# Kernel tuning notes

Hardware: AMD Instinct MI355X
Metric: run time of the kernel (lower is better)

The kernel has to match this reference:

```python
import math
import jax, jax.numpy as jnp
import numpy as np

N_HEADS = 16
NUM_BUCKETS = 32
MAX_DISTANCE = 128
ROTARY_BASE = 10000.0


def rotate_half(x):
    x1, x2 = jnp.split(x, 2, axis=-1)
    return jnp.concatenate((-x2, x1), axis=-1)


def rotary_freqs(T, dim):
    inv_freq = 1.0 / (ROTARY_BASE ** (jnp.arange(0, dim, 2, dtype=jnp.float32) / dim))
    t = jnp.arange(T, dtype=jnp.float32)
    freqs = jnp.einsum('i,j->ij', t, inv_freq)  # [T, dim/2]
    return jnp.concatenate((freqs, freqs), axis=-1)  # [T, dim]


def rel_pos_bucket_causal(rel_pos, num_buckets=NUM_BUCKETS, max_distance=MAX_DISTANCE):
    n = jnp.maximum(-rel_pos, 0)  # [T, T] int
    max_exact = num_buckets // 2
    is_small = n < max_exact
    n_safe = jnp.maximum(n, 1).astype(jnp.float32)
    val_if_large = max_exact + (
        jnp.log(n_safe / max_exact) / math.log(max_distance / max_exact) * (num_buckets - max_exact)
    ).astype(jnp.int32)
    val_if_large = jnp.minimum(val_if_large, num_buckets - 1)
    return jnp.where(is_small, n, val_if_large)


def setup_inputs() -> dict:
    key = jax.random.key(0)
    ks = jax.random.split(key, 10)
    B, T, C = 2, 2048, 1024
    s = 0.02
    return {
        'x':  jax.random.normal(ks[0], (B, T, C), dtype=jnp.float32),
        'Wq': jax.random.normal(ks[1], (C, C), dtype=jnp.float32) * s,
        'bq': jnp.zeros((C,), dtype=jnp.float32),
        'Wk': jax.random.normal(ks[2], (C, C), dtype=jnp.float32) * s,
        'bk': jnp.zeros((C,), dtype=jnp.float32),
        'Wv': jax.random.normal(ks[3], (C, C), dtype=jnp.float32) * s,
        'bv': jnp.zeros((C,), dtype=jnp.float32),
        'Wp': jax.random.normal(ks[4], (C, C), dtype=jnp.float32) * s,
        'bp': jnp.zeros((C,), dtype=jnp.float32),
        'rel_bias_table': jax.random.normal(ks[5], (NUM_BUCKETS, N_HEADS), dtype=jnp.float32) * s,
    }


def reference(x, Wq, bq, Wk, bk, Wv, bv, Wp, bp, rel_bias_table):
    B, T, C = x.shape
    H = N_HEADS
    D = C // H

    def heads(y):
        return y.reshape(B, T, H, D).transpose(0, 2, 1, 3)  # [B,H,T,D]

    q = heads(x @ Wq + bq)
    k = heads(x @ Wk + bk)
    v = heads(x @ Wv + bv)

    # rotary (use_xpos=False -> scale=1)
    freqs = rotary_freqs(T, D)  # [T, D]
    cos, sin = jnp.cos(freqs), jnp.sin(freqs)
    q = q * cos + rotate_half(q) * sin
    k = k * cos + rotate_half(k) * sin

    # relative position bias (causal, scale=1.0)
    pos = jnp.arange(T)
    rel_pos = pos[None, :] - pos[:, None]  # k_pos - q_pos
    bucket = rel_pos_bucket_causal(rel_pos)  # [T, T]
    bias = rel_bias_table[bucket]  # [T, T, H]
    bias = bias.transpose(2, 0, 1)  # [H, T, T]

    att = jnp.einsum('bhid,bhjd->bhij', q, k) + bias[None]
    att = att * (1.0 / math.sqrt(D))
    causal = pos[None, :] <= pos[:, None]  # tril mask [T, T]
    att = jnp.where(causal[None, None], att, -jnp.inf)
    att = jax.nn.softmax(att, axis=-1)

    y = jnp.einsum('bhij,bhjd->bhid', att, v)  # [B,H,T,D]
    y = y.transpose(0, 2, 1, 3).reshape(B, T, C)
    return y @ Wp + bp
```

## Files before the change

### kernel.cpp

```cpp
#include <hip/hip_runtime.h>
#include <hip/hip_bf16.h>
#include <math.h>

#define B_ 2
#define T_ 2048
#define C_ 1024
#define H_ 16
#define D_ 64
#define M_ (B_ * T_)
#define K_ 1024

#define SCALE2 0.18033688011112043f

typedef short bf16x8 __attribute__((ext_vector_type(8)));
typedef float f32x4  __attribute__((ext_vector_type(4)));
typedef unsigned int u32;

__device__ __forceinline__ float u2f(unsigned short u) {
    union { unsigned int i; float f; } v; v.i = ((unsigned int)u) << 16; return v.f;
}
__device__ __forceinline__ unsigned short f2b(float f) {
    __hip_bfloat16 h = __float2bfloat16(f);
    return *reinterpret_cast<unsigned short*>(&h);
}
__device__ __forceinline__ u32 pack_bf16_rnd(float a, float b) {
    const u32 au = __float_as_uint(a) + 0x8000u;
    const u32 bu = __float_as_uint(b) + 0x8000u;
    return __builtin_amdgcn_perm(bu, au, 0x07060302u);
}
__device__ __forceinline__ void load_lds16(const void* g, void* l) {
    __builtin_amdgcn_global_load_lds(
        (const __attribute__((address_space(1))) u32*)g,
        (__attribute__((address_space(3))) u32*)l, 16, 0, 0);
}

__global__ __launch_bounds__(256) void prep(
    const float* __restrict__ x,
    const float* __restrict__ W0, const float* __restrict__ W1,
    const float* __restrict__ W2, const float* __restrict__ W3,
    const float* __restrict__ tbl,
    unsigned short* __restrict__ xb,
    unsigned short* __restrict__ T0, unsigned short* __restrict__ T1,
    unsigned short* __restrict__ T2, unsigned short* __restrict__ T3,
    float* __restrict__ dtab, float2* __restrict__ trig)
{
    __shared__ __align__(16) unsigned short tile[64][72];
    const int bx = blockIdx.x;
    const int tid = threadIdx.x;

    if (bx < 2048) {
        const int idx = bx * 256 + tid;
        const float4 a = reinterpret_cast<const float4*>(x)[idx * 2];
        const float4 b = reinterpret_cast<const float4*>(x)[idx * 2 + 1];
        unsigned short t[8] = {f2b(a.x), f2b(a.y), f2b(a.z), f2b(a.w),
                               f2b(b.x), f2b(b.y), f2b(b.z), f2b(b.w)};
        reinterpret_cast<bf16x8*>(xb)[idx] = *reinterpret_cast<const bf16x8*>(t);
    } else if (bx < 3072) {
        const int w = bx - 2048;
        const int z = w >> 8;
        const int rem = w & 255;
        const int k0 = (rem & 15) * 64, n0 = (rem >> 4) * 64;
        const float* W = z == 0 ? W0 : z == 1 ? W1 : z == 2 ? W2 : W3;
        unsigned short* Wt = z == 0 ? T0 : z == 1 ? T1 : z == 2 ? T2 : T3;

        #pragma unroll
        for (int it = 0; it < 4; ++it) {
            const int idx = it * 256 + tid;
            const int r = idx >> 4, c = (idx & 15) * 4;
            const float4 w4 = *reinterpret_cast<const float4*>(W + (size_t)(k0 + r) * C_ + n0 + c);
            tile[r][c + 0] = f2b(w4.x); tile[r][c + 1] = f2b(w4.y);
            tile[r][c + 2] = f2b(w4.z); tile[r][c + 3] = f2b(w4.w);
        }
        __syncthreads();
        #pragma unroll
        for (int it = 0; it < 2; ++it) {
            const int idx = it * 256 + tid;
            const int nc = idx >> 3, kc = (idx & 7) * 8;
            unsigned short tmp[8];
            #pragma unroll
            for (int e = 0; e < 8; ++e) tmp[e] = tile[kc + e][nc];
            *reinterpret_cast<bf16x8*>(Wt + (size_t)(n0 + nc) * K_ + k0 + kc) =
                *reinterpret_cast<const bf16x8*>(tmp);
        }
    } else {
        const int idx = (bx - 3072) * 256 + tid;
        if (idx < H_ * T_) {
            const int h = idx >> 11, n = idx & (T_ - 1);
            int bucket;
            if (n < 16) bucket = n;
            else {
                int vb = 16 + (int)(log2f((float)n * 0.0625f) * (16.0f / 3.0f));
                bucket = vb < 31 ? vb : 31;
            }
            dtab[idx] = tbl[bucket * H_ + h] * SCALE2;
        }
        const int t = idx >> 5, j = idx & 31;
        const float inv = exp2f(-(float)j * (13.287712379549449f / 32.0f));
        const float ang = (float)t * inv;
        trig[idx] = make_float2(cosf(ang), sinf(ang));
    }
}

__device__ __forceinline__ void gemm_core(
    const unsigned short* __restrict__ A, const unsigned short* __restrict__ Bt,
    const float* __restrict__ bias, const float2* __restrict__ trig,
    float rot_scale, float* __restrict__ outf,
    unsigned short* __restrict__ outb, int mode)
{
    __shared__ __align__(16) unsigned short As[128 * 32];
    __shared__ __align__(16) unsigned short Bs[128 * 32];

    const int tid = threadIdx.x;
    const int wid = tid >> 6, lane = tid & 63;
    const int l16 = lane & 15, quad = lane >> 4;
    const int wm = wid >> 1, wn = wid & 1;
    const int m0 = blockIdx.y * 128, n0 = blockIdx.x * 128;

    f32x4 acc[4][4];
    #pragma unroll
    for (int i = 0; i < 4; ++i)
        #pragma unroll
        for (int j = 0; j < 4; ++j) acc[i][j] = (f32x4){0.f, 0.f, 0.f, 0.f};

    char* AsB = (char*)As;
    char* BsB = (char*)Bs;

    for (int k0 = 0; k0 < K_; k0 += 32) {
        __syncthreads();
        #pragma unroll
        for (int it = 0; it < 2; ++it) {
            const int idx = it * 256 + tid;
            const int row = idx >> 2, ch = (idx & 3) * 8;
            const int ldso = it * 4096 + wid * 1024;
            load_lds16(A + (size_t)(m0 + row) * K_ + k0 + ch, AsB + ldso);
            load_lds16(Bt + (size_t)(n0 + row) * K_ + k0 + ch, BsB + ldso);
        }
        __syncthreads();

        bf16x8 af[4], bf[4];
        #pragma unroll
        for (int i = 0; i < 4; ++i) {
            af[i] = *reinterpret_cast<const bf16x8*>(&As[(wm * 64 + i * 16 + l16) * 32 + quad * 8]);
            bf[i] = *reinterpret_cast<const bf16x8*>(&Bs[(wn * 64 + i * 16 + l16) * 32 + quad * 8]);
        }
        #pragma unroll
        for (int i = 0; i < 4; ++i)
            #pragma unroll
            for (int j = 0; j < 4; ++j)
                acc[i][j] = __builtin_amdgcn_mfma_f32_16x16x32_bf16(af[i], bf[j], acc[i][j], 0, 0, 0);
    }

    if (mode == 1) {
        #pragma unroll
        for (int i = 0; i < 4; ++i) {
            const int mb = m0 + wm * 64 + i * 16 + quad * 4;
            const int bb = mb >> 11, tb = mb & (T_ - 1);
            #pragma unroll
            for (int jc = 0; jc < 2; ++jc) {
                const int n_lo = n0 + wn * 64 + jc * 16 + l16;
                const int h = n_lo >> 6, d = n_lo & 63;
                const float bv_lo = bias[n_lo], bv_hi = bias[n_lo + 32];
                unsigned short* po = outb + (((size_t)bb * H_ + h) * T_ + tb) * D_ + d;
                #pragma unroll
                for (int r = 0; r < 4; ++r) {
                    const float2 cs = trig[(tb + r) * 32 + d];
                    const float a = acc[i][jc][r] + bv_lo;
                    const float b = acc[i][jc + 2][r] + bv_hi;
                    po[(size_t)r * D_]      = f2b((a * cs.x - b * cs.y) * rot_scale);
                    po[(size_t)r * D_ + 32] = f2b((b * cs.x + a * cs.y) * rot_scale);
                }
            }
        }
        return;
    }

    #pragma unroll
    for (int i = 0; i < 4; ++i) {
        const int mb = m0 + wm * 64 + i * 16 + quad * 4;
        #pragma unroll
        for (int j = 0; j < 4; ++j) {
            const int n = n0 + wn * 64 + j * 16 + l16;
            const float bv = bias[n];
            if (mode == 2) {
                const int bb = mb >> 11, t = mb & (T_ - 1);
                const int h = n >> 6, d = n & 63;
                uint2 w;
                w.x = pack_bf16_rnd(acc[i][j][0] + bv, acc[i][j][1] + bv);
                w.y = pack_bf16_rnd(acc[i][j][2] + bv, acc[i][j][3] + bv);
                *reinterpret_cast<uint2*>(
                    outb + (((size_t)bb * H_ + h) * D_ + d) * T_ + t) = w;
            } else {
                #pragma unroll
                for (int r = 0; r < 4; ++r)
                    outf[(size_t)(mb + r) * C_ + n] = acc[i][j][r] + bv;
            }
        }
    }
}

__global__ __launch_bounds__(256) void gemm_qkv(
    const unsigned short* __restrict__ A,
    const unsigned short* __restrict__ Wq, const unsigned short* __restrict__ Wk,
    const unsigned short* __restrict__ Wv,
    const float* __restrict__ bq, const float* __restrict__ bk,
    const float* __restrict__ bv, const float2* __restrict__ trig,
    unsigned short* __restrict__ Qo, unsigned short* __restrict__ Ko,
    unsigned short* __restrict__ Vto)
{
    const int z = blockIdx.z;
    const unsigned short* Bt = z == 0 ? Wq : z == 1 ? Wk : Wv;
    const float* bias = z == 0 ? bq : z == 1 ? bk : bv;
    unsigned short* outb = z == 0 ? Qo : z == 1 ? Ko : Vto;
    const float rs = z == 0 ? SCALE2 : 1.0f;
    gemm_core(A, Bt, bias, trig, rs, nullptr, outb, z == 2 ? 2 : 1);
}

__global__ __launch_bounds__(256) void gemm_proj(
    const unsigned short* __restrict__ A, const unsigned short* __restrict__ Bt,
    const float* __restrict__ bias, float* __restrict__ outf)
{
    gemm_core(A, Bt, bias, nullptr, 1.0f, outf, nullptr, 0);
}

__global__ __launch_bounds__(256) void flash_attn(
    const unsigned short* __restrict__ Q, const unsigned short* __restrict__ K,
    const unsigned short* __restrict__ Vt, const float* __restrict__ dtab,
    unsigned short* __restrict__ Y)
{
    __shared__ __align__(16) unsigned short Ks[64][72];
    __shared__ __align__(16) unsigned short Vs[64][72];
    __shared__ __align__(16) unsigned short Ps[4][16][72];
    __shared__ float bias_ls[64 + T_];

    const int bh = blockIdx.y;
    const int qt = (int)((blockIdx.x + blockIdx.y) & 31);
    const int h = bh & (H_ - 1), b = bh >> 4;
    const int tid = threadIdx.x;
    const int wid = tid >> 6, lane = tid & 63;
    const int l16 = lane & 15, quad = lane >> 4;
    const size_t base = (size_t)bh * T_ * D_;
    const size_t vbase = (size_t)bh * D_ * T_;
    const int q0 = qt * 64;

    if (tid < 64) bias_ls[tid] = -INFINITY;
    for (int ii = tid; ii < q0 + 64; ii += 256) bias_ls[64 + ii] = dtab[h * T_ + ii];

    bf16x8 ones;
    #pragma unroll
    for (int e = 0; e < 8; ++e) ones[e] = (short)0x3F80;

    const int arow = q0 + wid * 16 + l16;
    const int crow = q0 + wid * 16 + quad * 4;
    const int nbase = crow - l16 * 4;

    const int sr0 = tid >> 3,         sch0 = (tid & 7) * 8;
    const int sr1 = (tid + 256) >> 3, sch1 = ((tid + 256) & 7) * 8;

    bf16x8 qf[2];
    qf[0] = *reinterpret_cast<const bf16x8*>(Q + base + (size_t)arow * D_ + quad * 8);
    qf[1] = *reinterpret_cast<const bf16x8*>(Q + base + (size_t)arow * D_ + 32 + quad * 8);

    bf16x8 kr[2], vr[2];
    kr[0] = *reinterpret_cast<const bf16x8*>(K + base + (size_t)sr0 * D_ + sch0);
    kr[1] = *reinterpret_cast<const bf16x8*>(K + base + (size_t)sr1 * D_ + sch1);
    vr[0] = *reinterpret_cast<const bf16x8*>(Vt + vbase + (size_t)sr0 * T_ + sch0);
    vr[1] = *reinterpret_cast<const bf16x8*>(Vt + vbase + (size_t)sr1 * T_ + sch1);

    f32x4 o[4], ol;
    #pragma unroll
    for (int c = 0; c < 4; ++c) o[c] = (f32x4){0.f, 0.f, 0.f, 0.f};
    ol = (f32x4){0.f, 0.f, 0.f, 0.f};

    for (int kt = 0; kt <= qt; ++kt) {
        const int j0 = kt * 64;
        __syncthreads();

        *reinterpret_cast<bf16x8*>(&Ks[sr0][sch0]) = kr[0];
        *reinterpret_cast<bf16x8*>(&Ks[sr1][sch1]) = kr[1];
        *reinterpret_cast<bf16x8*>(&Vs[sr0][sch0]) = vr[0];
        *reinterpret_cast<bf16x8*>(&Vs[sr1][sch1]) = vr[1];
        __syncthreads();

        if (kt < qt) {
            const int j1 = j0 + 64;
            kr[0] = *reinterpret_cast<const bf16x8*>(K + base + (size_t)(j1 + sr0) * D_ + sch0);
            kr[1] = *reinterpret_cast<const bf16x8*>(K + base + (size_t)(j1 + sr1) * D_ + sch1);
            vr[0] = *reinterpret_cast<const bf16x8*>(Vt + vbase + (size_t)sr0 * T_ + j1 + sch0);
            vr[1] = *reinterpret_cast<const bf16x8*>(Vt + vbase + (size_t)sr1 * T_ + j1 + sch1);
        }

        f32x4 sc[4];
        #pragma unroll
        for (int c = 0; c < 4; ++c) sc[c] = (f32x4){0.f, 0.f, 0.f, 0.f};
        #pragma unroll
        for (int c = 0; c < 4; ++c) {
            #pragma unroll
            for (int s = 0; s < 2; ++s) {
                bf16x8 kf = *reinterpret_cast<const bf16x8*>(
                    &Ks[l16 * 4 + c][s * 32 + quad * 8]);
                sc[c] = __builtin_amdgcn_mfma_f32_16x16x32_bf16(qf[s], kf, sc[c], 0, 0, 0);
            }
        }

        #pragma unroll
        for (int r = 0; r < 4; ++r) {
            const float* bp0 = &bias_ls[64 + nbase - j0 + r];
            const float p0 = exp2f(sc[0][r] + bp0[0]);
            const float p1 = exp2f(sc[1][r] + bp0[-1]);
            const float p2 = exp2f(sc[2][r] + bp0[-2]);
            const float p3 = exp2f(sc[3][r] + bp0[-3]);
            uint2 w;
            w.x = pack_bf16_rnd(p0, p1);
            w.y = pack_bf16_rnd(p2, p3);
            *reinterpret_cast<uint2*>(&Ps[wid][quad * 4 + r][l16 * 4]) = w;
        }

        #pragma unroll
        for (int s = 0; s < 2; ++s) {
            bf16x8 pf = *reinterpret_cast<const bf16x8*>(&Ps[wid][l16][s * 32 + quad * 8]);
            #pragma unroll
            for (int c = 0; c < 4; ++c) {
                bf16x8 vf = *reinterpret_cast<const bf16x8*>(&Vs[c * 16 + l16][s * 32 + quad * 8]);
                o[c] = __builtin_amdgcn_mfma_f32_16x16x32_bf16(pf, vf, o[c], 0, 0, 0);
            }
            ol = __builtin_amdgcn_mfma_f32_16x16x32_bf16(pf, ones, ol, 0, 0, 0);
        }
    }

    #pragma unroll
    for (int r = 0; r < 4; ++r) {
        const int i = crow + r;
        const float invl = 1.0f / ol[r];
        #pragma unroll
        for (int c = 0; c < 4; ++c)
            Y[((size_t)b * T_ + i) * C_ + h * D_ + c * 16 + l16] = f2b(o[c][r] * invl);
    }
}

extern "C" void kernel_launch(void* const* d_in, const int* in_sizes, int n_in,
                              void* d_out, int out_size, void* d_ws, size_t ws_size,
                              hipStream_t stream)
{
    const float* x   = (const float*)d_in[0];
    const float* Wq  = (const float*)d_in[1];
    const float* bq  = (const float*)d_in[2];
    const float* Wk  = (const float*)d_in[3];
    const float* bk  = (const float*)d_in[4];
    const float* Wv  = (const float*)d_in[5];
    const float* bv  = (const float*)d_in[6];
    const float* Wp  = (const float*)d_in[7];
    const float* bp  = (const float*)d_in[8];
    const float* tbl = (const float*)d_in[9];
    float* out = (float*)d_out;

    const size_t n1 = (size_t)B_ * H_ * T_ * D_;
    const size_t nW = (size_t)C_ * C_;
    unsigned short* xb  = (unsigned short*)d_ws;
    unsigned short* Wqt = xb + (size_t)M_ * K_;
    unsigned short* Wkt = Wqt + nW;
    unsigned short* Wvt = Wkt + nW;
    unsigned short* Wpt = Wvt + nW;
    unsigned short* Qb  = Wpt + nW;
    unsigned short* Kb  = Qb + n1;
    unsigned short* Vtb = Kb + n1;
    unsigned short* Yb  = Vtb + n1;
    float* dtab = (float*)(Yb + n1);
    float2* trig = (float2*)(dtab + H_ * T_);

    const dim3 blk(256);

    prep<<<dim3(3328), blk, 0, stream>>>(x, Wq, Wk, Wv, Wp, tbl,
                                         xb, Wqt, Wkt, Wvt, Wpt, dtab, trig);

    gemm_qkv<<<dim3(C_ / 128, M_ / 128, 3), blk, 0, stream>>>(
        xb, Wqt, Wkt, Wvt, bq, bk, bv, trig, Qb, Kb, Vtb);

    flash_attn<<<dim3(32, B_ * H_), blk, 0, stream>>>(Qb, Kb, Vtb, dtab, Yb);

    gemm_proj<<<dim3(C_ / 128, M_ / 128), blk, 0, stream>>>(Yb, Wpt, bp, out);
}
```

Baseline: 212.8 us.

## Pair causal query tiles per block and fold bias into MFMA accumulator

Each attention block now handles two query tiles (qt and 31-qt), so every block does the same amount of causal work and the grid shrinks from 32 to 16 blocks per head. The relative-position bias is loaded as vectors and used to initialise the QK^T accumulator, which removes the per-element bias adds before exp2. s_setprio is raised around the MFMA sections. The cost is fewer blocks (512) and therefore less parallelism, plus a serial second pass within each block that starts by reloading the first K/V tile.

After: 213.6 us. No clear change (+0.4%).

```diff
diff --git a/kernel.cpp b/kernel.cpp
--- a/kernel.cpp
+++ b/kernel.cpp
@@ -230,35 +230,28 @@
     __shared__ __align__(16) unsigned short Ks[64][72];
     __shared__ __align__(16) unsigned short Vs[64][72];
     __shared__ __align__(16) unsigned short Ps[4][16][72];
-    __shared__ float bias_ls[64 + T_];
+    __shared__ __align__(16) float bias_ls[64 + T_];
 
     const int bh = blockIdx.y;
-    const int qt = (int)((blockIdx.x + blockIdx.y) & 31);
     const int h = bh & (H_ - 1), b = bh >> 4;
     const int tid = threadIdx.x;
     const int wid = tid >> 6, lane = tid & 63;
     const int l16 = lane & 15, quad = lane >> 4;
     const size_t base = (size_t)bh * T_ * D_;
     const size_t vbase = (size_t)bh * D_ * T_;
-    const int q0 = qt * 64;
+
+    const int qta = (int)((blockIdx.x + blockIdx.y) & 15);
+    const int qtb = 31 - qta;
 
     if (tid < 64) bias_ls[tid] = -INFINITY;
-    for (int ii = tid; ii < q0 + 64; ii += 256) bias_ls[64 + ii] = dtab[h * T_ + ii];
+    for (int ii = tid; ii < qtb * 64 + 64; ii += 256) bias_ls[64 + ii] = dtab[h * T_ + ii];
 
     bf16x8 ones;
     #pragma unroll
     for (int e = 0; e < 8; ++e) ones[e] = (short)0x3F80;
 
-    const int arow = q0 + wid * 16 + l16;
-    const int crow = q0 + wid * 16 + quad * 4;
-    const int nbase = crow - l16 * 4;
-
     const int sr0 = tid >> 3,         sch0 = (tid & 7) * 8;
     const int sr1 = (tid + 256) >> 3, sch1 = ((tid + 256) & 7) * 8;
-
-    bf16x8 qf[2];
-    qf[0] = *reinterpret_cast<const bf16x8*>(Q + base + (size_t)arow * D_ + quad * 8);
-    qf[1] = *reinterpret_cast<const bf16x8*>(Q + base + (size_t)arow * D_ + 32 + quad * 8);
 
     bf16x8 kr[2], vr[2];
     kr[0] = *reinterpret_cast<const bf16x8*>(K + base + (size_t)sr0 * D_ + sch0);
@@ -266,74 +259,102 @@
     vr[0] = *reinterpret_cast<const bf16x8*>(Vt + vbase + (size_t)sr0 * T_ + sch0);
     vr[1] = *reinterpret_cast<const bf16x8*>(Vt + vbase + (size_t)sr1 * T_ + sch1);
 
-    f32x4 o[4], ol;
-    #pragma unroll
-    for (int c = 0; c < 4; ++c) o[c] = (f32x4){0.f, 0.f, 0.f, 0.f};
-    ol = (f32x4){0.f, 0.f, 0.f, 0.f};
-
-    for (int kt = 0; kt <= qt; ++kt) {
-        const int j0 = kt * 64;
-        __syncthreads();
-
-        *reinterpret_cast<bf16x8*>(&Ks[sr0][sch0]) = kr[0];
-        *reinterpret_cast<bf16x8*>(&Ks[sr1][sch1]) = kr[1];
-        *reinterpret_cast<bf16x8*>(&Vs[sr0][sch0]) = vr[0];
-        *reinterpret_cast<bf16x8*>(&Vs[sr1][sch1]) = vr[1];
-        __syncthreads();
-
-        if (kt < qt) {
-            const int j1 = j0 + 64;
-            kr[0] = *reinterpret_cast<const bf16x8*>(K + base + (size_t)(j1 + sr0) * D_ + sch0);
-            kr[1] = *reinterpret_cast<const bf16x8*>(K + base + (size_t)(j1 + sr1) * D_ + sch1);
-            vr[0] = *reinterpret_cast<const bf16x8*>(Vt + vbase + (size_t)sr0 * T_ + j1 + sch0);
-            vr[1] = *reinterpret_cast<const bf16x8*>(Vt + vbase + (size_t)sr1 * T_ + j1 + sch1);
-        }
-
-        f32x4 sc[4];
-        #pragma unroll
-        for (int c = 0; c < 4; ++c) sc[c] = (f32x4){0.f, 0.f, 0.f, 0.f};
-        #pragma unroll
-        for (int c = 0; c < 4; ++c) {
+    for (int qi = 0; qi < 2; ++qi) {
+        const int qt = qi ? qta : qtb;
+        const int q0 = qt * 64;
+        const int arow = q0 + wid * 16 + l16;
+        const int crow = q0 + wid * 16 + quad * 4;
+        const int nbase = crow - l16 * 4;
+
+        bf16x8 qf[2];
+        qf[0] = *reinterpret_cast<const bf16x8*>(Q + base + (size_t)arow * D_ + quad * 8);
+        qf[1] = *reinterpret_cast<const bf16x8*>(Q + base + (size_t)arow * D_ + 32 + quad * 8);
+
+        f32x4 o[4], ol;
+        #pragma unroll
+        for (int c = 0; c < 4; ++c) o[c] = (f32x4){0.f, 0.f, 0.f, 0.f};
+        ol = (f32x4){0.f, 0.f, 0.f, 0.f};
+
+        for (int kt = 0; kt <= qt; ++kt) {
+            const int j0 = kt * 64;
+            __syncthreads();
+
+            *reinterpret_cast<bf16x8*>(&Ks[sr0][sch0]) = kr[0];
+            *reinterpret_cast<bf16x8*>(&Ks[sr1][sch1]) = kr[1];
+            *reinterpret_cast<bf16x8*>(&Vs[sr0][sch0]) = vr[0];
+            *reinterpret_cast<bf16x8*>(&Vs[sr1][sch1]) = vr[1];
+            __syncthreads();
+
+            if (kt < qt) {
+                const int j1 = j0 + 64;
+                kr[0] = *reinterpret_cast<const bf16x8*>(K + base + (size_t)(j1 + sr0) * D_ + sch0);
+                kr[1] = *reinterpret_cast<const bf16x8*>(K + base + (size_t)(j1 + sr1) * D_ + sch1);
+                vr[0] = *reinterpret_cast<const bf16x8*>(Vt + vbase + (size_t)sr0 * T_ + j1 + sch0);
+                vr[1] = *reinterpret_cast<const bf16x8*>(Vt + vbase + (size_t)sr1 * T_ + j1 + sch1);
+            } else if (qi == 0) {
+                kr[0] = *reinterpret_cast<const bf16x8*>(K + base + (size_t)sr0 * D_ + sch0);
+                kr[1] = *reinterpret_cast<const bf16x8*>(K + base + (size_t)sr1 * D_ + sch1);
+                vr[0] = *reinterpret_cast<const bf16x8*>(Vt + vbase + (size_t)sr0 * T_ + sch0);
+                vr[1] = *reinterpret_cast<const bf16x8*>(Vt + vbase + (size_t)sr1 * T_ + sch1);
+            }
+
+            const int d0 = nbase - j0;
+            const f32x4 blo = *reinterpret_cast<const f32x4*>(&bias_ls[60 + d0]);
+            const f32x4 bhi = *reinterpret_cast<const f32x4*>(&bias_ls[64 + d0]);
+
+            f32x4 sc[4];
+            #pragma unroll
+            for (int c = 0; c < 4; ++c) {
+                #pragma unroll
+                for (int r = 0; r < 4; ++r)
+                    sc[c][r] = (r >= c) ? bhi[r - c] : blo[4 + r - c];
+            }
+            __builtin_amdgcn_s_setprio(1);
+            #pragma unroll
+            for (int c = 0; c < 4; ++c) {
+                #pragma unroll
+                for (int s = 0; s < 2; ++s) {
+                    bf16x8 kf = *reinterpret_cast<const bf16x8*>(
+                        &Ks[l16 * 4 + c][s * 32 + quad * 8]);
+                    sc[c] = __builtin_amdgcn_mfma_f32_16x16x32_bf16(qf[s], kf, sc[c], 0, 0, 0);
+                }
+            }
+            __builtin_amdgcn_s_setprio(0);
+
+            #pragma unroll
+            for (int r = 0; r < 4; ++r) {
+                const float p0 = exp2f(sc[0][r]);
+                const float p1 = exp2f(sc[1][r]);
+                const float p2 = exp2f(sc[2][r]);
+                const float p3 = exp2f(sc[3][r]);
+                uint2 w;
+                w.x = pack_bf16_rnd(p0, p1);
+                w.y = pack_bf16_rnd(p2, p3);
+                *reinterpret_cast<uint2*>(&Ps[wid][quad * 4 + r][l16 * 4]) = w;
+            }
+
+            __builtin_amdgcn_s_setprio(1);
             #pragma unroll
             for (int s = 0; s < 2; ++s) {
-                bf16x8 kf = *reinterpret_cast<const bf16x8*>(
-                    &Ks[l16 * 4 + c][s * 32 + quad * 8]);
-                sc[c] = __builtin_amdgcn_mfma_f32_16x16x32_bf16(qf[s], kf, sc[c], 0, 0, 0);
-            }
+                bf16x8 pf = *reinterpret_cast<const bf16x8*>(&Ps[wid][l16][s * 32 + quad * 8]);
+                #pragma unroll
+                for (int c = 0; c < 4; ++c) {
+                    bf16x8 vf = *reinterpret_cast<const bf16x8*>(&Vs[c * 16 + l16][s * 32 + quad * 8]);
+                    o[c] = __builtin_amdgcn_mfma_f32_16x16x32_bf16(pf, vf, o[c], 0, 0, 0);
+                }
+                ol = __builtin_amdgcn_mfma_f32_16x16x32_bf16(pf, ones, ol, 0, 0, 0);
+            }
+            __builtin_amdgcn_s_setprio(0);
         }
 
         #pragma unroll
         for (int r = 0; r < 4; ++r) {
-            const float* bp0 = &bias_ls[64 + nbase - j0 + r];
-            const float p0 = exp2f(sc[0][r] + bp0[0]);
-            const float p1 = exp2f(sc[1][r] + bp0[-1]);
-            const float p2 = exp2f(sc[2][r] + bp0[-2]);
-            const float p3 = exp2f(sc[3][r] + bp0[-3]);
-            uint2 w;
-            w.x = pack_bf16_rnd(p0, p1);
-            w.y = pack_bf16_rnd(p2, p3);
-            *reinterpret_cast<uint2*>(&Ps[wid][quad * 4 + r][l16 * 4]) = w;
-        }
-
-        #pragma unroll
-        for (int s = 0; s < 2; ++s) {
-            bf16x8 pf = *reinterpret_cast<const bf16x8*>(&Ps[wid][l16][s * 32 + quad * 8]);
-            #pragma unroll
-            for (int c = 0; c < 4; ++c) {
-                bf16x8 vf = *reinterpret_cast<const bf16x8*>(&Vs[c * 16 + l16][s * 32 + quad * 8]);
-                o[c] = __builtin_amdgcn_mfma_f32_16x16x32_bf16(pf, vf, o[c], 0, 0, 0);
-            }
-            ol = __builtin_amdgcn_mfma_f32_16x16x32_bf16(pf, ones, ol, 0, 0, 0);
-        }
-    }
-
-    #pragma unroll
-    for (int r = 0; r < 4; ++r) {
-        const int i = crow + r;
-        const float invl = 1.0f / ol[r];
-        #pragma unroll
-        for (int c = 0; c < 4; ++c)
-            Y[((size_t)b * T_ + i) * C_ + h * D_ + c * 16 + l16] = f2b(o[c][r] * invl);
+            const int i = crow + r;
+            const float invl = 1.0f / ol[r];
+            #pragma unroll
+            for (int c = 0; c < 4; ++c)
+                Y[((size_t)b * T_ + i) * C_ + h * D_ + c * 16 + l16] = f2b(o[c][r] * invl);
+        }
     }
 }
 
@@ -375,7 +396,7 @@
     gemm_qkv<<<dim3(C_ / 128, M_ / 128, 3), blk, 0, stream>>>(
         xb, Wqt, Wkt, Wvt, bq, bk, bv, trig, Qb, Kb, Vtb);
 
-    flash_attn<<<dim3(32, B_ * H_), blk, 0, stream>>>(Qb, Kb, Vtb, dtab, Yb);
+    flash_attn<<<dim3(16, B_ * H_), blk, 0, stream>>>(Qb, Kb, Vtb, dtab, Yb);
 
     gemm_proj<<<dim3(C_ / 128, M_ / 128), blk, 0, stream>>>(Yb, Wpt, bp, out);
 }
```
